# Performance work log

Measured on AMD Instinct MI355X. Metric: run time of the kernel, lower is better.

## Reference

```python
import jax, jax.numpy as jnp
import numpy as np

LN_EPS = 1e-5

def sin_emb(coords, dim):
    # coords [..., 3] -> [..., dim]; dim split evenly over 3 axes, sin/cos halves
    per_axis = dim // 3
    half = per_axis // 2
    freqs = jnp.exp(-jnp.log(10000.0) * jnp.arange(half, dtype=coords.dtype) / max(half - 1, 1))
    ang = coords[..., None] * freqs  # [..., 3, half]
    emb = jnp.concatenate([jnp.sin(ang), jnp.cos(ang)], axis=-1)  # [..., 3, per_axis]
    return emb.reshape(coords.shape[:-1] + (dim,))

def layernorm(x, g, b):
    mu = jnp.mean(x, axis=-1, keepdims=True)
    var = jnp.mean((x - mu) ** 2, axis=-1, keepdims=True)
    return (x - mu) * jax.lax.rsqrt(var + LN_EPS) * g + b

def point_mlp(x, w, b, g, be, act):
    h = layernorm(x @ w + b, g, be)
    return jax.nn.gelu(h, approximate=False) if act else h

def query_ball_point(radius, nsample, xyz):
    # xyz [B,N,3] -> idx [B,N,nsample] (pad with first in-ball index, PointNet++ style)
    N = xyz.shape[1]
    sq = jnp.sum((xyz[:, :, None, :] - xyz[:, None, :, :]) ** 2, axis=-1)  # [B,N,N]
    idx0 = jnp.where(sq > radius * radius, N, jnp.arange(N)[None, None, :])
    idx = jnp.sort(idx0, axis=-1)[:, :, :nsample]
    return jnp.where(idx == N, idx[:, :, :1], idx)

def index_points(points, idx):
    # points [B,N,C], idx [B,S,K] -> [B,S,K,C]
    return jax.vmap(lambda p, i: p[i])(points, idx)

def setup_inputs() -> dict:
    key = jax.random.key(0)
    ks = jax.random.split(key, 20)
    B, N, C_stem, C_tok = 4, 4096, 64, 256
    C_in = C_stem + 3 + 24 + 96  # 187
    w = lambda k, i, o: jax.random.normal(k, (i, o), jnp.float32) * 0.02
    inp = {
        'xyz': jax.random.uniform(ks[0], (B, N, 3), jnp.float32),
        'point_feature': jax.random.normal(ks[1], (B, N, C_stem), jnp.float32),
        # scene_point_mlp
        'w1': w(ks[2], C_in, C_tok), 'b1': jnp.zeros((C_tok,)), 'g1': jnp.ones((C_tok,)), 'be1': jnp.zeros((C_tok,)),
        'w2': w(ks[3], C_tok, C_tok), 'b2': jnp.zeros((C_tok,)), 'g2': jnp.ones((C_tok,)), 'be2': jnp.zeros((C_tok,)),
        # scene_projection
        'pw1': w(ks[4], C_tok, C_tok), 'pb1': jnp.zeros((C_tok,)), 'pg1': jnp.ones((C_tok,)), 'pbe1': jnp.zeros((C_tok,)),
        'pw2': w(ks[5], C_tok, C_tok), 'pb2': jnp.zeros((C_tok,)), 'pg2': jnp.ones((C_tok,)), 'pbe2': jnp.zeros((C_tok,)),
    }
    return inp

def reference(xyz, point_feature, w1, b1, g1, be1, w2, b2, g2, be2,
              pw1, pb1, pg1, pbe1, pw2, pb2, pg2, pbe2):
    radius, K = 0.16, 32
    idx = query_ball_point(radius, K, xyz)                     # [B,N,K]
    grouped_xyz = index_points(xyz, idx)                       # [B,N,K,3]
    grouped_feature = index_points(point_feature, idx)         # [B,N,K,Cs]
    relative_xyz = grouped_xyz - xyz[:, :, None, :]            # [B,N,K,3]
    relative_position = sin_emb(relative_xyz, 24)              # [B,N,K,24]
    absolute_position = sin_emb(xyz, 96)                       # [B,N,96]
    B, N = xyz.shape[0], xyz.shape[1]
    absolute_position = jnp.broadcast_to(absolute_position[:, :, None, :], (B, N, K, 96))
    grouped_input = jnp.concatenate(
        (grouped_feature, relative_xyz, relative_position, absolute_position), axis=-1)
    h = point_mlp(grouped_input, w1, b1, g1, be1, True)
    h = point_mlp(h, w2, b2, g2, be2, False)
    scene_point_feature = jnp.max(h, axis=2)                   # [B,N,C]
    pooled = jnp.max(scene_point_feature, axis=1, keepdims=True)  # [B,1,C]
    t = point_mlp(pooled, pw1, pb1, pg1, pbe1, True)
    global_scene_token = point_mlp(t, pw2, pb2, pg2, pbe2, False)
    return global_scene_token
```

## Files before the change

kernel.cpp:

```cpp
#include <hip/hip_runtime.h>
#include <hip/hip_bf16.h>
#include <math.h>


#define LN_EPS 1e-5f

typedef __attribute__((ext_vector_type(8))) short bf16x8;
typedef __attribute__((ext_vector_type(4))) float f32x4;
typedef __attribute__((ext_vector_type(2))) unsigned int u32x2;
typedef __attribute__((ext_vector_type(4))) unsigned int u32x4;

#if __has_builtin(__builtin_amdgcn_rcpf)
#define FRCP(x) __builtin_amdgcn_rcpf(x)
#else
#define FRCP(x) (1.0f / (x))
#endif

__device__ __forceinline__ unsigned short f2bf(float f) {
    unsigned int x = __float_as_uint(f);
    return (unsigned short)((x + 0x7FFFu + ((x >> 16) & 1u)) >> 16);
}
__device__ __forceinline__ unsigned int pack2(float a, float b) {
    union { __hip_bfloat162 h; unsigned int u; } cvt;
    cvt.h = __float22bfloat162_rn(make_float2(a, b));
    return cvt.u;
}
__device__ __forceinline__ unsigned int fenc(float f) {
    unsigned int u = __float_as_uint(f);
    return (u & 0x80000000u) ? ~u : (u | 0x80000000u);
}
__device__ __forceinline__ float fdec(unsigned int u) {
    return __uint_as_float((u & 0x80000000u) ? (u & 0x7FFFFFFFu) : ~u);
}
__device__ __forceinline__ float gelu_fast(float x) {
    float x2 = x * x;
    float u = x * fmaf(0.0356774081f, x2, 0.7978845608f);
    float e = exp2f(u * -2.8853900818f);
    float r = FRCP(e + 1.0f);
    return x * r;
}
template<int CTRL>
__device__ __forceinline__ float dppadd(float s) {
    int v = __builtin_amdgcn_update_dpp(0, __float_as_int(s), CTRL, 0xF, 0xF, true);
    return s + __int_as_float(v);
}
__device__ __forceinline__ float rowsum16(float x) {
    x = dppadd<0x128>(x);
    x = dppadd<0x124>(x);
    x = dppadd<0x122>(x);
    x = dppadd<0x121>(x);
    return x;
}

__global__ __launch_bounds__(256) void k_prep(
    const float* __restrict__ w1, const float* __restrict__ w2,
    unsigned short* __restrict__ w2T, unsigned short* __restrict__ w1aT,
    unsigned short* __restrict__ w1cT, unsigned short* __restrict__ w1bT,
    unsigned int* __restrict__ pooled_r)
{
    int t = threadIdx.x, blk = blockIdx.x;
    if (blk < 16) {
        __shared__ unsigned short tile[64][65];
        int tr = blk >> 2, tc = blk & 3;
        #pragma unroll
        for (int rr = 0; rr < 16; ++rr) {
            int kl = rr * 4 + (t >> 6), nl = t & 63;
            tile[kl][nl] = f2bf(w2[(size_t)(tr * 64 + kl) * 256 + tc * 64 + nl]);
        }
        __syncthreads();
        #pragma unroll
        for (int rr = 0; rr < 16; ++rr) {
            int nl = rr * 4 + (t >> 6), kp = t & 63;
            int kl = (kp & 3) * 16 + (kp >> 2);
            w2T[(size_t)(tc * 64 + nl) * 256 + tr * 64 + kp] = tile[kl][nl];
        }
    } else if (blk < 20) {
        __shared__ unsigned short tile[64][65];
        int tc = blk - 16;
        #pragma unroll
        for (int rr = 0; rr < 16; ++rr) {
            int kl = rr * 4 + (t >> 6), nl = t & 63;
            tile[kl][nl] = f2bf(w1[(size_t)kl * 256 + tc * 64 + nl]);
        }
        __syncthreads();
        #pragma unroll
        for (int rr = 0; rr < 16; ++rr) {
            int nl = rr * 4 + (t >> 6), kl = t & 63;
            w1aT[(size_t)(tc * 64 + nl) * 64 + kl] = tile[kl][nl];
        }
    } else if (blk < 28) {
        __shared__ unsigned short tile[64][65];
        int idx = blk - 20;
        int tr2 = idx >> 2, tc = idx & 3;
        #pragma unroll
        for (int rr = 0; rr < 16; ++rr) {
            int kl = rr * 4 + (t >> 6), nl = t & 63;
            int k = tr2 * 64 + kl;
            float v = 0.f;
            if (k < 96) v = w1[(size_t)(91 + k) * 256 + tc * 64 + nl];
            tile[kl][nl] = f2bf(v);
        }
        __syncthreads();
        #pragma unroll
        for (int rr = 0; rr < 16; ++rr) {
            int nl = rr * 4 + (t >> 6), kl = t & 63;
            int k = tr2 * 64 + kl;
            if (k < 96)
                w1cT[(size_t)(tc * 64 + nl) * 96 + k] = tile[kl][nl];
        }
    } else if (blk == 28) {
        int n = t;
        #pragma unroll
        for (int k = 0; k < 32; ++k) {
            unsigned short v = 0;
            if (k < 27) v = f2bf(w1[(size_t)(64 + k) * 256 + n]);
            w1bT[(size_t)n * 32 + k] = v;
        }
    } else {
        unsigned int idv = fenc(-1e19f);
        for (int q = t; q < 8192; q += 256) pooled_r[q] = idv;
    }
}

__global__ __launch_bounds__(256) void k_pre(
    const float* __restrict__ xyz, const float* __restrict__ pf,
    const unsigned short* __restrict__ w1aT, const unsigned short* __restrict__ w1cT,
    const float* __restrict__ b1,
    float* __restrict__ U_p, float* __restrict__ V_p)
{
    __shared__ __align__(16) unsigned short ptile[64 * 72];
    __shared__ __align__(16) unsigned short etile[64 * 104];
    int tid = threadIdx.x, wv = tid >> 6, lane = tid & 63;
    int lo16 = lane & 15, quad = lane >> 4;
    int rows0 = blockIdx.x * 64;

    {
        int r = tid >> 2, seg = tid & 3;
        const f32x4* src = (const f32x4*)(pf + (size_t)(rows0 + r) * 64 + seg * 16);
        f32x4 v0 = src[0], v1 = src[1], v2 = src[2], v3 = src[3];
        u32x4 o0, o1;
        o0.x = pack2(v0.x, v0.y); o0.y = pack2(v0.z, v0.w);
        o0.z = pack2(v1.x, v1.y); o0.w = pack2(v1.z, v1.w);
        o1.x = pack2(v2.x, v2.y); o1.y = pack2(v2.z, v2.w);
        o1.z = pack2(v3.x, v3.y); o1.w = pack2(v3.z, v3.w);
        u32x4* dst = (u32x4*)&ptile[r * 72 + seg * 16];
        dst[0] = o0; dst[1] = o1;
    }
    {
        int r = tid & 63, grp = tid >> 6;
        float c0 = xyz[(size_t)(rows0 + r) * 3];
        float c1 = xyz[(size_t)(rows0 + r) * 3 + 1];
        float c2 = xyz[(size_t)(rows0 + r) * 3 + 2];
        #pragma unroll
        for (int q = 0; q < 12; ++q) {
            int pr = grp * 12 + q;
            float vals[2];
            #pragma unroll
            for (int qq = 0; qq < 2; ++qq) {
                int cc = pr * 2 + qq;
                int a = cc >> 5, wI = cc & 31;
                int jf = (wI < 16) ? wI : (wI - 16);
                float coord = (a == 0) ? c0 : ((a == 1) ? c1 : c2);
                float fr = __expf(-0.61402269146507894f * (float)jf);
                float ang = coord * fr;
                vals[qq] = (wI < 16) ? __sinf(ang) : __cosf(ang);
            }
            *(unsigned int*)&etile[r * 104 + 2 * pr] = pack2(vals[0], vals[1]);
        }
    }
    __syncthreads();

    f32x4 acc[4][4];
    #pragma unroll
    for (int mt = 0; mt < 4; ++mt)
        #pragma unroll
        for (int nt = 0; nt < 4; ++nt) acc[mt][nt] = (f32x4){0.f, 0.f, 0.f, 0.f};
    #pragma unroll
    for (int ks = 0; ks < 2; ++ks) {
        bf16x8 bfr[4];
        #pragma unroll
        for (int nt = 0; nt < 4; ++nt) {
            int n = wv * 64 + nt * 16 + lo16;
            bfr[nt] = *(const bf16x8*)&w1aT[(size_t)n * 64 + ks * 32 + quad * 8];
        }
        #pragma unroll
        for (int mt = 0; mt < 4; ++mt) {
            bf16x8 afr = *(const bf16x8*)&ptile[(mt * 16 + lo16) * 72 + ks * 32 + quad * 8];
            #pragma unroll
            for (int nt = 0; nt < 4; ++nt)
                acc[mt][nt] = __builtin_amdgcn_mfma_f32_16x16x32_bf16(
                    afr, bfr[nt], acc[mt][nt], 0, 0, 0);
        }
    }
    #pragma unroll
    for (int mt = 0; mt < 4; ++mt)
        #pragma unroll
        for (int reg = 0; reg < 4; ++reg) {
            f32x4 o = {acc[mt][0][reg], acc[mt][1][reg], acc[mt][2][reg], acc[mt][3][reg]};
            *(f32x4*)&U_p[(size_t)(rows0 + mt * 16 + quad * 4 + reg) * 256 + wv * 64 + lo16 * 4] = o;
        }

    {
        float b1f[4];
        #pragma unroll
        for (int nt = 0; nt < 4; ++nt) b1f[nt] = b1[wv * 64 + nt * 16 + lo16];
        #pragma unroll
        for (int mt = 0; mt < 4; ++mt)
            #pragma unroll
            for (int nt = 0; nt < 4; ++nt)
                #pragma unroll
                for (int reg = 0; reg < 4; ++reg) acc[mt][nt][reg] = b1f[nt];
    }
    #pragma unroll
    for (int ks = 0; ks < 3; ++ks) {
        bf16x8 bfr[4];
        #pragma unroll
        for (int nt = 0; nt < 4; ++nt) {
            int n = wv * 64 + nt * 16 + lo16;
            bfr[nt] = *(const bf16x8*)&w1cT[(size_t)n * 96 + ks * 32 + quad * 8];
        }
        #pragma unroll
        for (int mt = 0; mt < 4; ++mt) {
            bf16x8 afr = *(const bf16x8*)&etile[(mt * 16 + lo16) * 104 + ks * 32 + quad * 8];
            #pragma unroll
            for (int nt = 0; nt < 4; ++nt)
                acc[mt][nt] = __builtin_amdgcn_mfma_f32_16x16x32_bf16(
                    afr, bfr[nt], acc[mt][nt], 0, 0, 0);
        }
    }
    #pragma unroll
    for (int mt = 0; mt < 4; ++mt)
        #pragma unroll
        for (int reg = 0; reg < 4; ++reg) {
            f32x4 o = {acc[mt][0][reg], acc[mt][1][reg], acc[mt][2][reg], acc[mt][3][reg]};
            *(f32x4*)&V_p[(size_t)(rows0 + mt * 16 + quad * 4 + reg) * 256 + wv * 64 + lo16 * 4] = o;
        }
}

__global__ __launch_bounds__(512, 4) void k_main(
    const float* __restrict__ xyz,
    const unsigned short* __restrict__ w1bT, const unsigned short* __restrict__ w2T,
    const float* __restrict__ U_p, const float* __restrict__ V_p,
    const float* __restrict__ g1, const float* __restrict__ be1,
    const float* __restrict__ b2, const float* __restrict__ g2,
    const float* __restrict__ be2,
    unsigned int* __restrict__ pooled_r)
{
    __shared__ __align__(16) unsigned short smem[128 * 264];
    __shared__ unsigned long long bmask[4][64];
    __shared__ int   idxs[128];
    __shared__ float ctr[4][3];
    __shared__ float reds[128][4][2];
    __shared__ float musig[128][2];
    __shared__ unsigned int pool_s[256];
    unsigned short* rels = smem;
    unsigned short* h1s  = smem;

    const int N = 4096;
    int tid = threadIdx.x, wv = tid >> 6, lane = tid & 63;
    int lo16 = lane & 15, quad = lane >> 4;
    int wvM = wv >> 2, wvN = wv & 3;
    int b = blockIdx.x & 3;
    int i0 = (blockIdx.x >> 2) * 4;
    int rep = (blockIdx.x >> 2) & 7;
    size_t base = (size_t)b * N;
    const float* xb = xyz + base * 3;

    bf16x8 bfrR[4];
    #pragma unroll
    for (int nt = 0; nt < 4; ++nt) {
        int n = wvN * 64 + nt * 16 + lo16;
        bfrR[nt] = *(const bf16x8*)&w1bT[(size_t)n * 32 + quad * 8];
    }

    if (tid < 256) pool_s[tid] = fenc(-1e19f);
    if (tid < 12) { int p = tid / 3, a = tid - 3 * p; ctr[p][a] = xb[(i0 + p) * 3 + a]; }
    const double r2d = 0.16 * 0.16;
    float T = (float)r2d;
    if ((double)T > r2d) T = __uint_as_float(__float_as_uint(T) - 1u);
    {
        f32x4 cA = *(const f32x4*)(xb + (size_t)i0 * 3);
        f32x4 cB = *(const f32x4*)(xb + (size_t)i0 * 3 + 4);
        f32x4 cC = *(const f32x4*)(xb + (size_t)i0 * 3 + 8);
        float cx0 = cA.x, cy0 = cA.y, cz0 = cA.z;
        float cx1 = cA.w, cy1 = cB.x, cz1 = cB.y;
        float cx2 = cB.z, cy2 = cB.w, cz2 = cC.x;
        float cx3 = cC.y, cy3 = cC.z, cz3 = cC.w;
        #pragma unroll 2
        for (int i = 0; i < 8; ++i) {
            int chunk = wv * 8 + i;
            int j = chunk * 64 + lane;
            const float* pp = xb + (size_t)j * 3;
            float px = pp[0], py = pp[1], pz = pp[2];
            float dx0 = __fsub_rn(px, cx0), dy0 = __fsub_rn(py, cy0), dz0 = __fsub_rn(pz, cz0);
            float sq0 = __fadd_rn(__fadd_rn(__fmul_rn(dx0, dx0), __fmul_rn(dy0, dy0)),
                                  __fmul_rn(dz0, dz0));
            unsigned long long m0 = __ballot(sq0 <= T);
            float dx1 = __fsub_rn(px, cx1), dy1 = __fsub_rn(py, cy1), dz1 = __fsub_rn(pz, cz1);
            float sq1 = __fadd_rn(__fadd_rn(__fmul_rn(dx1, dx1), __fmul_rn(dy1, dy1)),
                                  __fmul_rn(dz1, dz1));
            unsigned long long m1 = __ballot(sq1 <= T);
            float dx2 = __fsub_rn(px, cx2), dy2 = __fsub_rn(py, cy2), dz2 = __fsub_rn(pz, cz2);
            float sq2 = __fadd_rn(__fadd_rn(__fmul_rn(dx2, dx2), __fmul_rn(dy2, dy2)),
                                  __fmul_rn(dz2, dz2));
            unsigned long long m2 = __ballot(sq2 <= T);
            float dx3 = __fsub_rn(px, cx3), dy3 = __fsub_rn(py, cy3), dz3 = __fsub_rn(pz, cz3);
            float sq3 = __fadd_rn(__fadd_rn(__fmul_rn(dx3, dx3), __fmul_rn(dy3, dy3)),
                                  __fmul_rn(dz3, dz3));
            unsigned long long m3 = __ballot(sq3 <= T);
            if (lane == 0) {
                bmask[0][chunk] = m0; bmask[1][chunk] = m1;
                bmask[2][chunk] = m2; bmask[3][chunk] = m3;
            }
        }
    }
    __syncthreads();
    if (wv < 4) {
        int p = wv;
        unsigned long long m = bmask[p][lane];
        int c = __popcll(m);
        int inc = c;
        #pragma unroll
        for (int d = 1; d <= 32; d <<= 1) {
            int v = __shfl_up(inc, d);
            if (lane >= d) inc += v;
        }
        int exc = inc - c;
        int total = __shfl(inc, 63);
        unsigned long long lm = __ballot(m != 0ull);
        int fl = __ffsll(lm) - 1;
        unsigned long long mf = (unsigned long long)__shfl((long long)m, fl);
        int firstj = fl * 64 + __ffsll(mf) - 1;
        unsigned long long mm = m;
        int t = 0;
        while (mm != 0ull && (exc + t) < 32) {
            int bpos = __ffsll(mm) - 1;
            idxs[p * 32 + exc + t] = lane * 64 + bpos;
            mm &= mm - 1; ++t;
        }
        if (lane >= total && lane < 32) idxs[p * 32 + lane] = firstj;
    }
    __syncthreads();

    {
        int r = tid & 127, part = tid >> 7;
        int p = r >> 5;
        int j = idxs[r];
        float rx = xb[j * 3]     - ctr[p][0];
        float ry = xb[j * 3 + 1] - ctr[p][1];
        float rz = xb[j * 3 + 2] - ctr[p][2];
        unsigned short* arow = &rels[r * 40];
        if (part == 0) {
            *(unsigned int*)&arow[0] = pack2(rx, ry);
            arow[2] = f2bf(rz);
            arow[27] = 0;
            *(u32x2*)&arow[28] = (u32x2){0u, 0u};
        } else {
            int a = part - 1;
            float cv = (a == 0) ? rx : ((a == 1) ? ry : rz);
            const float fr4[4] = {1.f, 0.046415888336127774f,
                                  0.0021544346900318843f, 1e-4f};
            float sn[4], cs[4];
            #pragma unroll
            for (int tt = 0; tt < 4; ++tt) {
                float ang = cv * fr4[tt];
                sn[tt] = __sinf(ang); cs[tt] = __cosf(ang);
            }
            arow[3 + a * 8 + 0] = f2bf(sn[0]); arow[3 + a * 8 + 1] = f2bf(sn[1]);
            arow[3 + a * 8 + 2] = f2bf(sn[2]); arow[3 + a * 8 + 3] = f2bf(sn[3]);
            arow[3 + a * 8 + 4] = f2bf(cs[0]); arow[3 + a * 8 + 5] = f2bf(cs[1]);
            arow[3 + a * 8 + 6] = f2bf(cs[2]); arow[3 + a * 8 + 7] = f2bf(cs[3]);
        }
    }
    __syncthreads();

    const int arow0 = wvM * 64;
    f32x4 acc[4][4];
    #pragma unroll
    for (int mt = 0; mt < 4; ++mt) {
        int cl = wvM * 2 + (mt >> 1);
        f32x4 vv = *(const f32x4*)&V_p[(size_t)(base + i0 + cl) * 256 + wvN * 64 + lo16 * 4];
        #pragma unroll
        for (int reg = 0; reg < 4; ++reg) {
            int r = arow0 + mt * 16 + quad * 4 + reg;
            int j = idxs[r];
            f32x4 uu = *(const f32x4*)&U_p[(size_t)(base + j) * 256 + wvN * 64 + lo16 * 4];
            #pragma unroll
            for (int nt = 0; nt < 4; ++nt) acc[mt][nt][reg] = uu[nt] + vv[nt];
        }
    }
    #pragma unroll
    for (int mt = 0; mt < 4; ++mt) {
        bf16x8 afr = *(const bf16x8*)&rels[(arow0 + mt * 16 + lo16) * 40 + quad * 8];
        #pragma unroll
        for (int nt = 0; nt < 4; ++nt)
            acc[mt][nt] = __builtin_amdgcn_mfma_f32_16x16x32_bf16(
                afr, bfrR[nt], acc[mt][nt], 0, 0, 0);
    }

    #pragma unroll
    for (int mt = 0; mt < 4; ++mt) {
        #pragma unroll
        for (int reg = 0; reg < 4; ++reg) {
            float s1 = 0.f, s2 = 0.f;
            #pragma unroll
            for (int nt = 0; nt < 4; ++nt) { float v = acc[mt][nt][reg]; s1 += v; s2 = fmaf(v, v, s2); }
            s1 = rowsum16(s1); s2 = rowsum16(s2);
            if (lo16 == 0) {
                int r = arow0 + mt * 16 + quad * 4 + reg;
                reds[r][wvN][0] = s1; reds[r][wvN][1] = s2;
            }
        }
    }
    __syncthreads();
    if (tid < 128) {
        int r = tid;
        float s1 = reds[r][0][0] + reds[r][1][0] + reds[r][2][0] + reds[r][3][0];
        float s2 = reds[r][0][1] + reds[r][1][1] + reds[r][2][1] + reds[r][3][1];
        float mu = s1 * (1.f / 256.f);
        float var = fmaxf(s2 * (1.f / 256.f) - mu * mu, 0.f);
        musig[r][0] = mu; musig[r][1] = rsqrtf(var + LN_EPS);
    }
    __syncthreads();
    {
        float g1f[4], be1f[4];
        #pragma unroll
        for (int nt = 0; nt < 4; ++nt) {
            int n = wvN * 64 + nt * 16 + lo16;
            g1f[nt] = g1[n]; be1f[nt] = be1[n];
        }
        #pragma unroll
        for (int mt = 0; mt < 4; ++mt) {
            #pragma unroll
            for (int reg = 0; reg < 4; ++reg) {
                int r = arow0 + mt * 16 + quad * 4 + reg;
                float mu = musig[r][0], rs = musig[r][1];
                float v0 = gelu_fast(fmaf((acc[mt][0][reg] - mu) * rs, g1f[0], be1f[0]));
                float v1 = gelu_fast(fmaf((acc[mt][1][reg] - mu) * rs, g1f[1], be1f[1]));
                float v2 = gelu_fast(fmaf((acc[mt][2][reg] - mu) * rs, g1f[2], be1f[2]));
                float v3 = gelu_fast(fmaf((acc[mt][3][reg] - mu) * rs, g1f[3], be1f[3]));
                u32x2 w; w.x = pack2(v0, v1); w.y = pack2(v2, v3);
                *(u32x2*)&h1s[r * 264 + wvN * 64 + lo16 * 4] = w;
            }
        }
    }
    __syncthreads();

    {
        float b2f[4];
        #pragma unroll
        for (int nt = 0; nt < 4; ++nt) b2f[nt] = b2[wvN * 64 + nt * 16 + lo16];
        #pragma unroll
        for (int mt = 0; mt < 4; ++mt)
            #pragma unroll
            for (int nt = 0; nt < 4; ++nt)
                #pragma unroll
                for (int reg = 0; reg < 4; ++reg) acc[mt][nt][reg] = b2f[nt];
    }
    for (int ks = 0; ks < 8; ++ks) {
        bf16x8 bfr[4], afr[4];
        #pragma unroll
        for (int nt = 0; nt < 4; ++nt) {
            int n = wvN * 64 + nt * 16 + lo16;
            bfr[nt] = *(const bf16x8*)&w2T[(size_t)n * 256 + ks * 32 + quad * 8];
        }
        #pragma unroll
        for (int mt = 0; mt < 4; ++mt)
            afr[mt] = *(const bf16x8*)&h1s[(arow0 + mt * 16 + lo16) * 264 + ks * 32 + quad * 8];
        #pragma unroll
        for (int mt = 0; mt < 4; ++mt)
            #pragma unroll
            for (int nt = 0; nt < 4; ++nt)
                acc[mt][nt] = __builtin_amdgcn_mfma_f32_16x16x32_bf16(
                    afr[mt], bfr[nt], acc[mt][nt], 0, 0, 0);
    }

    {
        #pragma unroll
        for (int mt = 0; mt < 4; ++mt) {
            #pragma unroll
            for (int reg = 0; reg < 4; ++reg) {
                float s1 = 0.f, s2 = 0.f;
                #pragma unroll
                for (int nt = 0; nt < 4; ++nt) { float v = acc[mt][nt][reg]; s1 += v; s2 = fmaf(v, v, s2); }
                s1 = rowsum16(s1); s2 = rowsum16(s2);
                if (lo16 == 0) {
                    int r = arow0 + mt * 16 + quad * 4 + reg;
                    reds[r][wvN][0] = s1; reds[r][wvN][1] = s2;
                }
            }
        }
        __syncthreads();
        if (tid < 128) {
            int r = tid;
            float s1 = reds[r][0][0] + reds[r][1][0] + reds[r][2][0] + reds[r][3][0];
            float s2 = reds[r][0][1] + reds[r][1][1] + reds[r][2][1] + reds[r][3][1];
            float mu = s1 * (1.f / 256.f);
            float var = fmaxf(s2 * (1.f / 256.f) - mu * mu, 0.f);
            musig[r][0] = mu; musig[r][1] = rsqrtf(var + LN_EPS);
        }
        __syncthreads();

        float g2f[4], be2f[4];
        #pragma unroll
        for (int nt = 0; nt < 4; ++nt) {
            int n = wvN * 64 + nt * 16 + lo16;
            g2f[nt] = g2[n]; be2f[nt] = be2[n];
        }
        float mx[4] = {-1e30f, -1e30f, -1e30f, -1e30f};
        #pragma unroll
        for (int mt = 0; mt < 4; ++mt) {
            #pragma unroll
            for (int reg = 0; reg < 4; ++reg) {
                int r = arow0 + mt * 16 + quad * 4 + reg;
                float mu = musig[r][0], rs = musig[r][1];
                #pragma unroll
                for (int nt = 0; nt < 4; ++nt) {
                    float v = fmaf((acc[mt][nt][reg] - mu) * rs, g2f[nt], be2f[nt]);
                    mx[nt] = fmaxf(mx[nt], v);
                }
            }
        }
        #pragma unroll
        for (int nt = 0; nt < 4; ++nt) {
            mx[nt] = fmaxf(mx[nt], __shfl_xor(mx[nt], 16));
            mx[nt] = fmaxf(mx[nt], __shfl_xor(mx[nt], 32));
        }
        if (quad == 0) {
            #pragma unroll
            for (int nt = 0; nt < 4; ++nt)
                atomicMax(&pool_s[wvN * 64 + nt * 16 + lo16], fenc(mx[nt]));
        }
    }
    __syncthreads();
    if (tid < 256)
        atomicMax(pooled_r + rep * 1024 + b * 256 + tid, pool_s[tid]);
}

__global__ __launch_bounds__(256) void k_final(
    const unsigned int* __restrict__ pooled_r,
    const float* __restrict__ pw1, const float* __restrict__ pb1,
    const float* __restrict__ pg1, const float* __restrict__ pbe1,
    const float* __restrict__ pw2, const float* __restrict__ pb2,
    const float* __restrict__ pg2, const float* __restrict__ pbe2,
    float* __restrict__ out)
{
    __shared__ float xw4[4][512];
    int tid = threadIdx.x, wv = tid >> 6, lane = tid & 63;
    int bb = wv;
    float* xw = xw4[wv];

    #pragma unroll
    for (int q = 0; q < 4; ++q) {
        int c = q * 64 + lane;
        unsigned int mv = pooled_r[bb * 256 + c];
        #pragma unroll
        for (int r = 1; r < 8; ++r) {
            unsigned int v = pooled_r[r * 1024 + bb * 256 + c];
            mv = (v > mv) ? v : mv;
        }
        xw[c] = fdec(mv);
    }

    float a1[4];
    #pragma unroll
    for (int q = 0; q < 4; ++q) a1[q] = pb1[q * 64 + lane];
    #pragma unroll 4
    for (int k = 0; k < 256; ++k) {
        float xv = xw[k];
        const float* wr = pw1 + (size_t)k * 256 + lane;
        #pragma unroll
        for (int q = 0; q < 4; ++q) a1[q] = fmaf(xv, wr[q * 64], a1[q]);
    }
    float s1 = a1[0] + a1[1] + a1[2] + a1[3];
    float s2 = fmaf(a1[0], a1[0], fmaf(a1[1], a1[1],
               fmaf(a1[2], a1[2], a1[3] * a1[3])));
    s1 = rowsum16(s1); s2 = rowsum16(s2);
    s1 += __shfl_xor(s1, 16); s2 += __shfl_xor(s2, 16);
    s1 += __shfl_xor(s1, 32); s2 += __shfl_xor(s2, 32);
    float mu = s1 * (1.f / 256.f);
    float rs = rsqrtf(fmaxf(s2 * (1.f / 256.f) - mu * mu, 0.f) + LN_EPS);
    #pragma unroll
    for (int q = 0; q < 4; ++q) {
        int c = q * 64 + lane;
        xw[256 + c] = gelu_fast(fmaf((a1[q] - mu) * rs, pg1[c], pbe1[c]));
    }

    float a2[4];
    #pragma unroll
    for (int q = 0; q < 4; ++q) a2[q] = pb2[q * 64 + lane];
    #pragma unroll 4
    for (int k = 0; k < 256; ++k) {
        float xv = xw[256 + k];
        const float* wr = pw2 + (size_t)k * 256 + lane;
        #pragma unroll
        for (int q = 0; q < 4; ++q) a2[q] = fmaf(xv, wr[q * 64], a2[q]);
    }
    s1 = a2[0] + a2[1] + a2[2] + a2[3];
    s2 = fmaf(a2[0], a2[0], fmaf(a2[1], a2[1],
         fmaf(a2[2], a2[2], a2[3] * a2[3])));
    s1 = rowsum16(s1); s2 = rowsum16(s2);
    s1 += __shfl_xor(s1, 16); s2 += __shfl_xor(s2, 16);
    s1 += __shfl_xor(s1, 32); s2 += __shfl_xor(s2, 32);
    mu = s1 * (1.f / 256.f);
    rs = rsqrtf(fmaxf(s2 * (1.f / 256.f) - mu * mu, 0.f) + LN_EPS);
    #pragma unroll
    for (int q = 0; q < 4; ++q) {
        int c = q * 64 + lane;
        out[bb * 256 + c] = fmaf((a2[q] - mu) * rs, pg2[c], pbe2[c]);
    }
}

extern "C" void kernel_launch(void* const* d_in, const int* in_sizes, int n_in,
                              void* d_out, int out_size, void* d_ws, size_t ws_size,
                              hipStream_t stream)
{
    char* ws = (char*)d_ws;
    unsigned short* w2T      = (unsigned short*)ws;
    unsigned short* w1aT     = (unsigned short*)(ws + (128u << 10));
    unsigned short* w1cT     = (unsigned short*)(ws + (160u << 10));
    unsigned short* w1bT     = (unsigned short*)(ws + (208u << 10));
    unsigned int*   pooled_r = (unsigned int*)(ws + (224u << 10));
    float*          U_p      = (float*)(ws + (256u << 10));
    float*          V_p      = (float*)(ws + (256u << 10) + (16u << 20));

    const float* xyz = (const float*)d_in[0];
    const float* pf  = (const float*)d_in[1];
    const float* w1  = (const float*)d_in[2];
    const float* b1  = (const float*)d_in[3];

    k_prep<<<30, 256, 0, stream>>>(w1, (const float*)d_in[6],
                                   w2T, w1aT, w1cT, w1bT, pooled_r);
    k_pre<<<256, 256, 0, stream>>>(xyz, pf, w1aT, w1cT, b1, U_p, V_p);
    k_main<<<4096, 512, 0, stream>>>(xyz, w1bT, w2T, U_p, V_p,
                                     (const float*)d_in[4], (const float*)d_in[5],
                                     (const float*)d_in[7], (const float*)d_in[8],
                                     (const float*)d_in[9], pooled_r);
    k_final<<<1, 256, 0, stream>>>(pooled_r,
                                   (const float*)d_in[10], (const float*)d_in[11],
                                   (const float*)d_in[12], (const float*)d_in[13],
                                   (const float*)d_in[14], (const float*)d_in[15],
                                   (const float*)d_in[16], (const float*)d_in[17],
                                   (float*)d_out);
}
```

Baseline: 402.0 us.

## Spread pre-GEMM, pooled replicas and final MLP across more blocks

```diff
diff --git a/kernel.cpp b/kernel.cpp
--- a/kernel.cpp
+++ b/kernel.cpp
@@ -118,7 +118,7 @@
         }
     } else {
         unsigned int idv = fenc(-1e19f);
-        for (int q = t; q < 8192; q += 256) pooled_r[q] = idv;
+        for (int q = t; q < 32768; q += 256) pooled_r[q] = idv;
     }
 }
 
@@ -128,113 +128,80 @@
     const float* __restrict__ b1,
     float* __restrict__ U_p, float* __restrict__ V_p)
 {
-    __shared__ __align__(16) unsigned short ptile[64 * 72];
-    __shared__ __align__(16) unsigned short etile[64 * 104];
+    __shared__ __align__(16) unsigned short ptile[16 * 72];
+    __shared__ __align__(16) unsigned short etile[16 * 104];
     int tid = threadIdx.x, wv = tid >> 6, lane = tid & 63;
     int lo16 = lane & 15, quad = lane >> 4;
-    int rows0 = blockIdx.x * 64;
-
-    {
-        int r = tid >> 2, seg = tid & 3;
-        const f32x4* src = (const f32x4*)(pf + (size_t)(rows0 + r) * 64 + seg * 16);
-        f32x4 v0 = src[0], v1 = src[1], v2 = src[2], v3 = src[3];
-        u32x4 o0, o1;
-        o0.x = pack2(v0.x, v0.y); o0.y = pack2(v0.z, v0.w);
-        o0.z = pack2(v1.x, v1.y); o0.w = pack2(v1.z, v1.w);
-        o1.x = pack2(v2.x, v2.y); o1.y = pack2(v2.z, v2.w);
-        o1.z = pack2(v3.x, v3.y); o1.w = pack2(v3.z, v3.w);
-        u32x4* dst = (u32x4*)&ptile[r * 72 + seg * 16];
-        dst[0] = o0; dst[1] = o1;
-    }
-    {
-        int r = tid & 63, grp = tid >> 6;
-        float c0 = xyz[(size_t)(rows0 + r) * 3];
-        float c1 = xyz[(size_t)(rows0 + r) * 3 + 1];
-        float c2 = xyz[(size_t)(rows0 + r) * 3 + 2];
-        #pragma unroll
-        for (int q = 0; q < 12; ++q) {
-            int pr = grp * 12 + q;
-            float vals[2];
-            #pragma unroll
-            for (int qq = 0; qq < 2; ++qq) {
-                int cc = pr * 2 + qq;
-                int a = cc >> 5, wI = cc & 31;
-                int jf = (wI < 16) ? wI : (wI - 16);
-                float coord = (a == 0) ? c0 : ((a == 1) ? c1 : c2);
-                float fr = __expf(-0.61402269146507894f * (float)jf);
-                float ang = coord * fr;
-                vals[qq] = (wI < 16) ? __sinf(ang) : __cosf(ang);
-            }
-            *(unsigned int*)&etile[r * 104 + 2 * pr] = pack2(vals[0], vals[1]);
-        }
-    }
-    __syncthreads();
-
-    f32x4 acc[4][4];
-    #pragma unroll
-    for (int mt = 0; mt < 4; ++mt)
-        #pragma unroll
-        for (int nt = 0; nt < 4; ++nt) acc[mt][nt] = (f32x4){0.f, 0.f, 0.f, 0.f};
+    int rows0 = blockIdx.x * 16;
+
+    {
+        int r = tid >> 4, seg = tid & 15;
+        f32x4 v = *(const f32x4*)(pf + (size_t)(rows0 + r) * 64 + seg * 4);
+        u32x2 o; o.x = pack2(v.x, v.y); o.y = pack2(v.z, v.w);
+        *(u32x2*)&ptile[r * 72 + seg * 4] = o;
+    }
+    #pragma unroll
+    for (int q = 0; q < 3; ++q) {
+        int item = q * 256 + tid;
+        int r = item / 48, pr = item - 48 * r;
+        float vals[2];
+        #pragma unroll
+        for (int qq = 0; qq < 2; ++qq) {
+            int cc = pr * 2 + qq;
+            int a = cc >> 5, wI = cc & 31;
+            int jf = (wI < 16) ? wI : (wI - 16);
+            float coord = xyz[(size_t)(rows0 + r) * 3 + a];
+            float fr = __expf(-0.61402269146507894f * (float)jf);
+            float ang = coord * fr;
+            vals[qq] = (wI < 16) ? __sinf(ang) : __cosf(ang);
+        }
+        *(unsigned int*)&etile[r * 104 + 2 * pr] = pack2(vals[0], vals[1]);
+    }
+    __syncthreads();
+
+    f32x4 acc[4];
+    #pragma unroll
+    for (int nt = 0; nt < 4; ++nt) acc[nt] = (f32x4){0.f, 0.f, 0.f, 0.f};
     #pragma unroll
     for (int ks = 0; ks < 2; ++ks) {
-        bf16x8 bfr[4];
+        bf16x8 afr = *(const bf16x8*)&ptile[lo16 * 72 + ks * 32 + quad * 8];
         #pragma unroll
         for (int nt = 0; nt < 4; ++nt) {
             int n = wv * 64 + nt * 16 + lo16;
-            bfr[nt] = *(const bf16x8*)&w1aT[(size_t)n * 64 + ks * 32 + quad * 8];
-        }
-        #pragma unroll
-        for (int mt = 0; mt < 4; ++mt) {
-            bf16x8 afr = *(const bf16x8*)&ptile[(mt * 16 + lo16) * 72 + ks * 32 + quad * 8];
-            #pragma unroll
-            for (int nt = 0; nt < 4; ++nt)
-                acc[mt][nt] = __builtin_amdgcn_mfma_f32_16x16x32_bf16(
-                    afr, bfr[nt], acc[mt][nt], 0, 0, 0);
-        }
-    }
-    #pragma unroll
-    for (int mt = 0; mt < 4; ++mt)
-        #pragma unroll
-        for (int reg = 0; reg < 4; ++reg) {
-            f32x4 o = {acc[mt][0][reg], acc[mt][1][reg], acc[mt][2][reg], acc[mt][3][reg]};
-            *(f32x4*)&U_p[(size_t)(rows0 + mt * 16 + quad * 4 + reg) * 256 + wv * 64 + lo16 * 4] = o;
-        }
+            bf16x8 bfr = *(const bf16x8*)&w1aT[(size_t)n * 64 + ks * 32 + quad * 8];
+            acc[nt] = __builtin_amdgcn_mfma_f32_16x16x32_bf16(afr, bfr, acc[nt], 0, 0, 0);
+        }
+    }
+    #pragma unroll
+    for (int reg = 0; reg < 4; ++reg) {
+        f32x4 o = {acc[0][reg], acc[1][reg], acc[2][reg], acc[3][reg]};
+        *(f32x4*)&U_p[(size_t)(rows0 + quad * 4 + reg) * 256 + wv * 64 + lo16 * 4] = o;
+    }
 
     {
         float b1f[4];
         #pragma unroll
         for (int nt = 0; nt < 4; ++nt) b1f[nt] = b1[wv * 64 + nt * 16 + lo16];
         #pragma unroll
-        for (int mt = 0; mt < 4; ++mt)
-            #pragma unroll
-            for (int nt = 0; nt < 4; ++nt)
-                #pragma unroll
-                for (int reg = 0; reg < 4; ++reg) acc[mt][nt][reg] = b1f[nt];
+        for (int nt = 0; nt < 4; ++nt)
+            #pragma unroll
+            for (int reg = 0; reg < 4; ++reg) acc[nt][reg] = b1f[nt];
     }
     #pragma unroll
     for (int ks = 0; ks < 3; ++ks) {
-        bf16x8 bfr[4];
+        bf16x8 afr = *(const bf16x8*)&etile[lo16 * 104 + ks * 32 + quad * 8];
         #pragma unroll
         for (int nt = 0; nt < 4; ++nt) {
             int n = wv * 64 + nt * 16 + lo16;
-            bfr[nt] = *(const bf16x8*)&w1cT[(size_t)n * 96 + ks * 32 + quad * 8];
-        }
-        #pragma unroll
-        for (int mt = 0; mt < 4; ++mt) {
-            bf16x8 afr = *(const bf16x8*)&etile[(mt * 16 + lo16) * 104 + ks * 32 + quad * 8];
-            #pragma unroll
-            for (int nt = 0; nt < 4; ++nt)
-                acc[mt][nt] = __builtin_amdgcn_mfma_f32_16x16x32_bf16(
-                    afr, bfr[nt], acc[mt][nt], 0, 0, 0);
-        }
-    }
-    #pragma unroll
-    for (int mt = 0; mt < 4; ++mt)
-        #pragma unroll
-        for (int reg = 0; reg < 4; ++reg) {
-            f32x4 o = {acc[mt][0][reg], acc[mt][1][reg], acc[mt][2][reg], acc[mt][3][reg]};
-            *(f32x4*)&V_p[(size_t)(rows0 + mt * 16 + quad * 4 + reg) * 256 + wv * 64 + lo16 * 4] = o;
-        }
+            bf16x8 bfr = *(const bf16x8*)&w1cT[(size_t)n * 96 + ks * 32 + quad * 8];
+            acc[nt] = __builtin_amdgcn_mfma_f32_16x16x32_bf16(afr, bfr, acc[nt], 0, 0, 0);
+        }
+    }
+    #pragma unroll
+    for (int reg = 0; reg < 4; ++reg) {
+        f32x4 o = {acc[0][reg], acc[1][reg], acc[2][reg], acc[3][reg]};
+        *(f32x4*)&V_p[(size_t)(rows0 + quad * 4 + reg) * 256 + wv * 64 + lo16 * 4] = o;
+    }
 }
 
 __global__ __launch_bounds__(512, 4) void k_main(
@@ -262,7 +229,7 @@
     int wvM = wv >> 2, wvN = wv & 3;
     int b = blockIdx.x & 3;
     int i0 = (blockIdx.x >> 2) * 4;
-    int rep = (blockIdx.x >> 2) & 7;
+    int rep = (blockIdx.x >> 2) & 31;
     size_t base = (size_t)b * N;
     const float* xb = xyz + base * 3;
 
@@ -545,70 +512,54 @@
     const float* __restrict__ pg2, const float* __restrict__ pbe2,
     float* __restrict__ out)
 {
-    __shared__ float xw4[4][512];
-    int tid = threadIdx.x, wv = tid >> 6, lane = tid & 63;
-    int bb = wv;
-    float* xw = xw4[wv];
-
-    #pragma unroll
-    for (int q = 0; q < 4; ++q) {
-        int c = q * 64 + lane;
-        unsigned int mv = pooled_r[bb * 256 + c];
-        #pragma unroll
-        for (int r = 1; r < 8; ++r) {
-            unsigned int v = pooled_r[r * 1024 + bb * 256 + c];
+    __shared__ float xw[256], xh[256];
+    __shared__ float lred[2][4];
+    int tid = threadIdx.x, wv = tid >> 6;
+    int bb = blockIdx.x;
+
+    {
+        unsigned int mv = pooled_r[bb * 256 + tid];
+        #pragma unroll
+        for (int r = 1; r < 32; ++r) {
+            unsigned int v = pooled_r[r * 1024 + bb * 256 + tid];
             mv = (v > mv) ? v : mv;
         }
-        xw[c] = fdec(mv);
-    }
-
-    float a1[4];
-    #pragma unroll
-    for (int q = 0; q < 4; ++q) a1[q] = pb1[q * 64 + lane];
-    #pragma unroll 4
-    for (int k = 0; k < 256; ++k) {
-        float xv = xw[k];
-        const float* wr = pw1 + (size_t)k * 256 + lane;
-        #pragma unroll
-        for (int q = 0; q < 4; ++q) a1[q] = fmaf(xv, wr[q * 64], a1[q]);
-    }
-    float s1 = a1[0] + a1[1] + a1[2] + a1[3];
-    float s2 = fmaf(a1[0], a1[0], fmaf(a1[1], a1[1],
-               fmaf(a1[2], a1[2], a1[3] * a1[3])));
+        xw[tid] = fdec(mv);
+    }
+    __syncthreads();
+
+    float a1 = pb1[tid];
+    #pragma unroll 8
+    for (int k = 0; k < 256; ++k)
+        a1 = fmaf(xw[k], pw1[(size_t)k * 256 + tid], a1);
+    float s1 = a1, s2 = a1 * a1;
     s1 = rowsum16(s1); s2 = rowsum16(s2);
     s1 += __shfl_xor(s1, 16); s2 += __shfl_xor(s2, 16);
     s1 += __shfl_xor(s1, 32); s2 += __shfl_xor(s2, 32);
+    if ((tid & 63) == 0) { lred[0][wv] = s1; lred[1][wv] = s2; }
+    __syncthreads();
+    s1 = lred[0][0] + lred[0][1] + lred[0][2] + lred[0][3];
+    s2 = lred[1][0] + lred[1][1] + lred[1][2] + lred[1][3];
     float mu = s1 * (1.f / 256.f);
     float rs = rsqrtf(fmaxf(s2 * (1.f / 256.f) - mu * mu, 0.f) + LN_EPS);
-    #pragma unroll
-    for (int q = 0; q < 4; ++q) {
-        int c = q * 64 + lane;
-        xw[256 + c] = gelu_fast(fmaf((a1[q] - mu) * rs, pg1[c], pbe1[c]));
-    }
-
-    float a2[4];
-    #pragma unroll
-    for (int q = 0; q < 4; ++q) a2[q] = pb2[q * 64 + lane];
-    #pragma unroll 4
-    for (int k = 0; k < 256; ++k) {
-        float xv = xw[256 + k];
-        const float* wr = pw2 + (size_t)k * 256 + lane;
-        #pragma unroll
-        for (int q = 0; q < 4; ++q) a2[q] = fmaf(xv, wr[q * 64], a2[q]);
-    }
-    s1 = a2[0] + a2[1] + a2[2] + a2[3];
-    s2 = fmaf(a2[0], a2[0], fmaf(a2[1], a2[1],
-         fmaf(a2[2], a2[2], a2[3] * a2[3])));
+    xh[tid] = gelu_fast(fmaf((a1 - mu) * rs, pg1[tid], pbe1[tid]));
+    __syncthreads();
+
+    float a2 = pb2[tid];
+    #pragma unroll 8
+    for (int k = 0; k < 256; ++k)
+        a2 = fmaf(xh[k], pw2[(size_t)k * 256 + tid], a2);
+    s1 = a2; s2 = a2 * a2;
     s1 = rowsum16(s1); s2 = rowsum16(s2);
     s1 += __shfl_xor(s1, 16); s2 += __shfl_xor(s2, 16);
     s1 += __shfl_xor(s1, 32); s2 += __shfl_xor(s2, 32);
+    if ((tid & 63) == 0) { lred[0][wv] = s1; lred[1][wv] = s2; }
+    __syncthreads();
+    s1 = lred[0][0] + lred[0][1] + lred[0][2] + lred[0][3];
+    s2 = lred[1][0] + lred[1][1] + lred[1][2] + lred[1][3];
     mu = s1 * (1.f / 256.f);
     rs = rsqrtf(fmaxf(s2 * (1.f / 256.f) - mu * mu, 0.f) + LN_EPS);
-    #pragma unroll
-    for (int q = 0; q < 4; ++q) {
-        int c = q * 64 + lane;
-        out[bb * 256 + c] = fmaf((a2[q] - mu) * rs, pg2[c], pbe2[c]);
-    }
+    out[bb * 256 + tid] = fmaf((a2 - mu) * rs, pg2[tid], pbe2[tid]);
 }
 
 extern "C" void kernel_launch(void* const* d_in, const int* in_sizes, int n_in,
@@ -621,8 +572,8 @@
     unsigned short* w1cT     = (unsigned short*)(ws + (160u << 10));
     unsigned short* w1bT     = (unsigned short*)(ws + (208u << 10));
     unsigned int*   pooled_r = (unsigned int*)(ws + (224u << 10));
-    float*          U_p      = (float*)(ws + (256u << 10));
-    float*          V_p      = (float*)(ws + (256u << 10) + (16u << 20));
+    float*          U_p      = (float*)(ws + (512u << 10));
+    float*          V_p      = (float*)(ws + (512u << 10) + (16u << 20));
 
     const float* xyz = (const float*)d_in[0];
     const float* pf  = (const float*)d_in[1];
@@ -631,12 +582,12 @@
 
     k_prep<<<30, 256, 0, stream>>>(w1, (const float*)d_in[6],
                                    w2T, w1aT, w1cT, w1bT, pooled_r);
-    k_pre<<<256, 256, 0, stream>>>(xyz, pf, w1aT, w1cT, b1, U_p, V_p);
+    k_pre<<<1024, 256, 0, stream>>>(xyz, pf, w1aT, w1cT, b1, U_p, V_p);
     k_main<<<4096, 512, 0, stream>>>(xyz, w1bT, w2T, U_p, V_p,
                                      (const float*)d_in[4], (const float*)d_in[5],
                                      (const float*)d_in[7], (const float*)d_in[8],
                                      (const float*)d_in[9], pooled_r);
-    k_final<<<1, 256, 0, stream>>>(pooled_r,
+    k_final<<<4, 256, 0, stream>>>(pooled_r,
                                    (const float*)d_in[10], (const float*)d_in[11],
                                    (const float*)d_in[12], (const float*)d_in[13],
                                    (const float*)d_in[14], (const float*)d_in[15],
```

Measured after the change: 390.1 us (median of 3 runs). -3.0%, faster.
